# Kernel optimization log

Hardware: AMD Instinct MI355X
Metric: run time of the kernel (lower is better)

Reference implementation:

```python
import jax, jax.numpy as jnp
import numpy as np

B, N, DIM = 8, 512, 512
HEADS, HD = 8, 64          # head_dim = dim // num_heads
E_ATT = 24                 # num_attn_experts, top-k = HEADS
E_FFD, K_FFD = 16, 2       # num_ffd_experts, top-k = ffd_heads
HID = 1024                 # int(dim*mlp_ratio) // ffd_heads = 2048 // 2
TASKS = 9
SWITCH_W, Z_W = 0.01, 0.001
SCALE = HD ** -0.5


def layer_norm(x, g, b, eps=1e-5):
    m = x.mean(-1, keepdims=True)
    v = ((x - m) ** 2).mean(-1, keepdims=True)
    return (x - m) * jax.lax.rsqrt(v + eps) * g + b


def top_k_gating(xf, w_gate, k, n_experts):
    # xf: [T, C], w_gate: [C, E]  (eval mode: no noise)
    logits = xf @ w_gate                                      # [T, E]
    probs = jax.nn.softmax(logits, axis=-1)
    vals, idx = jax.lax.top_k(probs, k)                       # [T, k]
    denom = jax.lax.stop_gradient(vals.sum(-1, keepdims=True) + 1e-6)
    gates = vals / denom                                      # renormalized top-k gates
    one_hot = jax.nn.one_hot(idx, n_experts, dtype=probs.dtype)  # [T, k, E]
    freqs = jax.lax.stop_gradient(one_hot.sum((0, 1)))        # tokens per expert [E]
    p_sum = probs.sum(0)
    switch = n_experts * jnp.sum((p_sum / p_sum.sum()) * (freqs / freqs.sum()))
    z = jnp.mean(jax.nn.logsumexp(logits, axis=-1) ** 2)
    loss = SWITCH_W * switch + Z_W * z
    return gates, one_hot, loss


def _forward(x, task_bh, norm1_g, norm1_b, gate_att, wq, wo_att, kv_w, kv_b,
             norm2_g, norm2_b, gate_mlp, wi, bi, wo_mlp, bo):
    Bs, Ns, C = x.shape
    T = Bs * Ns
    # ---- MoE task attention (MoA-style: experts produce query heads) ----
    x1 = layer_norm(x, norm1_g, norm1_b).reshape(T, C)
    gates, oh, loss1 = top_k_gating(x1, gate_att[task_bh], HEADS, E_ATT)
    # map: per-slot expert query projection (not gate-weighted)
    q_all = jnp.einsum('tc,ech->teh', x1, wq)                 # [T, E, hd]
    q = jnp.einsum('teh,tke->tkh', q_all, oh)                 # [T, H, hd]
    q = q.reshape(Bs, Ns, HEADS, HD)
    kv = x1 @ kv_w + kv_b                                     # shared single-head k,v
    k_, v_ = jnp.split(kv.reshape(Bs, Ns, 2 * HD), 2, axis=-1)
    attn = jnp.einsum('bihd,bjd->bhij', q, k_) * SCALE
    attn = jax.nn.softmax(attn, axis=-1)
    o = jnp.einsum('bhij,bjd->bihd', attn, v_).reshape(T, HEADS, HD)
    # reduce: gate-weighted per-expert output projection
    comb = jnp.einsum('tkd,tk,tke->ted', o, gates, oh)        # [T, E, hd]
    y = jnp.einsum('ted,edc->tc', comb, wo_att).reshape(Bs, Ns, C)
    x = x + y
    # ---- MoE task MLP ----
    x2 = layer_norm(x, norm2_g, norm2_b).reshape(T, C)
    gates2, oh2, loss2 = top_k_gating(x2, gate_mlp[task_bh], K_FFD, E_FFD)
    g_dense = jnp.einsum('tk,tke->te', gates2, oh2)           # sparse gates densified [T,E]
    h = jax.nn.gelu(jnp.einsum('tc,ech->teh', x2, wi) + bi, approximate=False)
    y2 = jnp.einsum('teh,te,ehc->tc', h, g_dense, wo_mlp) + g_dense @ bo
    x = x + y2.reshape(Bs, Ns, C)
    return x, loss1 + loss2


def setup_inputs() -> dict:
    key = jax.random.key(0)
    ks = jax.random.split(key, 8)
    s = 0.02
    return {
        'x': jax.random.normal(ks[0], (B, N, DIM), jnp.float32),
        'task_bh': 3,
        'norm1_g': jnp.ones((DIM,), jnp.float32),
        'norm1_b': jnp.zeros((DIM,), jnp.float32),
        'gate_att': jax.random.normal(ks[1], (TASKS, DIM, E_ATT), jnp.float32) * s,
        'wq': jax.random.normal(ks[2], (E_ATT, DIM, HD), jnp.float32) * s,
        'wo_att': jax.random.normal(ks[3], (E_ATT, HD, DIM), jnp.float32) * s,
        'kv_w': jax.random.normal(ks[4], (DIM, 2 * HD), jnp.float32) * s,
        'kv_b': jnp.zeros((2 * HD,), jnp.float32),
        'norm2_g': jnp.ones((DIM,), jnp.float32),
        'norm2_b': jnp.zeros((DIM,), jnp.float32),
        'gate_mlp': jax.random.normal(ks[5], (TASKS, DIM, E_FFD), jnp.float32) * s,
        'wi': jax.random.normal(ks[6], (E_FFD, DIM, HID), jnp.float32) * s,
        'bi': jnp.zeros((E_FFD, HID), jnp.float32),
        'wo_mlp': jax.random.normal(ks[7], (E_FFD, HID, DIM), jnp.float32) * s,
        'bo': jnp.zeros((E_FFD, DIM), jnp.float32),
    }


def reference(x, task_bh, norm1_g, norm1_b, gate_att, wq, wo_att, kv_w, kv_b,
              norm2_g, norm2_b, gate_mlp, wi, bi, wo_mlp, bo):
    return _forward(x, task_bh, norm1_g, norm1_b, gate_att, wq, wo_att, kv_w, kv_b,
                    norm2_g, norm2_b, gate_mlp, wi, bi, wo_mlp, bo)
```

## Files before the change

### kernel.cpp

```cpp
#include <hip/hip_runtime.h>
#include <math.h>

namespace {

constexpr int T   = 4096;
constexpr int C   = 512;
constexpr int NB  = 8;
constexpr int NS  = 512;
constexpr int HD  = 64;
constexpr int KA  = 8;
constexpr int EA  = 24;
constexpr int EF  = 16;
constexpr int KF  = 2;
constexpr int HID = 1024;

typedef __attribute__((ext_vector_type(8))) short bf16x8;
typedef __attribute__((ext_vector_type(4))) float f32x4;

__device__ inline unsigned short f2bf(float f) {
  unsigned u = __float_as_uint(f);
  return (unsigned short)((u + 0x7FFFu + ((u >> 16) & 1u)) >> 16);
}
__device__ inline float bf2f(unsigned short u) {
  return __uint_as_float((unsigned)u << 16);
}

template <int E, int TS>
__device__ inline bool tile_from_counts(const int* counts, int tile, int& e_out, int& t0_out) {
  int e = 0;
  for (; e < E; e++) {
    int nt = (counts[e] + TS - 1) / TS;
    if (tile < nt) break;
    tile -= nt;
  }
  e_out = e; t0_out = tile * TS;
  return e < E;
}

template <int E, int K, bool RESID>
__global__ __launch_bounds__(1024) void ln_gate_kernel(
    const float* __restrict__ in, const unsigned short* __restrict__ yslot,
    float* __restrict__ resid_out,
    const float* __restrict__ g, const float* __restrict__ b,
    const float* __restrict__ gate_all, const int* __restrict__ task,
    unsigned short* __restrict__ outb,
    float* __restrict__ probs, float* __restrict__ lse_out,
    float* __restrict__ gates, int* __restrict__ idxs) {
  constexpr int TPB = 16;
  constexpr int XSS = 516;
  int tid = threadIdx.x, lane = tid & 63, wv = tid >> 6;
  int tb = blockIdx.x * TPB;
  __shared__ float xs[TPB][XSS];
  __shared__ float lp[2][TPB][E];
  __shared__ __align__(16) float Wt[E][XSS];
  const float* W = gate_all + (size_t)task[0] * C * E;
  for (int i = tid; i < C * E; i += 1024) {
    int c = i / E, e = i - c * E;
    Wt[e][c] = W[i];
  }
  int c0 = lane * 8;
  const float4 g0 = *(const float4*)&g[c0], g1 = *(const float4*)&g[c0 + 4];
  const float4 b0 = *(const float4*)&b[c0], b1 = *(const float4*)&b[c0 + 4];
  {
    int tt = wv;
    int t = tb + tt;
    const float* row = in + (size_t)t * C + c0;
    float4 v0 = *(const float4*)&row[0];
    float4 v1 = *(const float4*)&row[4];
    if (RESID) {
      #pragma unroll
      for (int k = 0; k < KA; k++) {
        uint4 u = *(const uint4*)&yslot[((size_t)t * KA + k) * C + c0];
        const unsigned short* us = (const unsigned short*)&u;
        v0.x += bf2f(us[0]); v0.y += bf2f(us[1]); v0.z += bf2f(us[2]); v0.w += bf2f(us[3]);
        v1.x += bf2f(us[4]); v1.y += bf2f(us[5]); v1.z += bf2f(us[6]); v1.w += bf2f(us[7]);
      }
      *(float4*)&resid_out[(size_t)t * C + c0]     = v0;
      *(float4*)&resid_out[(size_t)t * C + c0 + 4] = v1;
    }
    float s = (v0.x + v0.y) + (v0.z + v0.w) + (v1.x + v1.y) + (v1.z + v1.w);
    #pragma unroll
    for (int m = 1; m < 64; m <<= 1) s += __shfl_xor(s, m);
    float mean = s * (1.f / C);
    float d[8] = {v0.x - mean, v0.y - mean, v0.z - mean, v0.w - mean,
                  v1.x - mean, v1.y - mean, v1.z - mean, v1.w - mean};
    float vv = 0.f;
    #pragma unroll
    for (int j = 0; j < 8; j++) vv += d[j] * d[j];
    #pragma unroll
    for (int m = 1; m < 64; m <<= 1) vv += __shfl_xor(vv, m);
    float r = rsqrtf(vv * (1.f / C) + 1e-5f);
    float o[8];
    o[0] = d[0] * r * g0.x + b0.x; o[1] = d[1] * r * g0.y + b0.y;
    o[2] = d[2] * r * g0.z + b0.z; o[3] = d[3] * r * g0.w + b0.w;
    o[4] = d[4] * r * g1.x + b1.x; o[5] = d[5] * r * g1.y + b1.y;
    o[6] = d[6] * r * g1.z + b1.z; o[7] = d[7] * r * g1.w + b1.w;
    *(ushort4*)&outb[(size_t)t * C + c0] =
        make_ushort4(f2bf(o[0]), f2bf(o[1]), f2bf(o[2]), f2bf(o[3]));
    *(ushort4*)&outb[(size_t)t * C + c0 + 4] =
        make_ushort4(f2bf(o[4]), f2bf(o[5]), f2bf(o[6]), f2bf(o[7]));
    #pragma unroll
    for (int j = 0; j < 8; j++) xs[tt][c0 + j] = o[j];
  }
  __syncthreads();
  if (tid < TPB * E * 2) {
    int half = tid / (TPB * E);
    int rem = tid - half * (TPB * E);
    int e = rem % E, tt = rem / E;
    int cb = half * (C / 2);
    float a0 = 0.f, a1 = 0.f, a2 = 0.f, a3 = 0.f;
    float a4 = 0.f, a5 = 0.f, a6 = 0.f, a7 = 0.f;
    #pragma unroll 4
    for (int c = cb; c < cb + C / 2; c += 8) {
      const float4 xv0 = *(const float4*)&xs[tt][c];
      const float4 xv1 = *(const float4*)&xs[tt][c + 4];
      const float4 wv0 = *(const float4*)&Wt[e][c];
      const float4 wv1 = *(const float4*)&Wt[e][c + 4];
      a0 += xv0.x * wv0.x; a1 += xv0.y * wv0.y;
      a2 += xv0.z * wv0.z; a3 += xv0.w * wv0.w;
      a4 += xv1.x * wv1.x; a5 += xv1.y * wv1.y;
      a6 += xv1.z * wv1.z; a7 += xv1.w * wv1.w;
    }
    lp[half][tt][e] = ((a0 + a1) + (a2 + a3)) + ((a4 + a5) + (a6 + a7));
  }
  __syncthreads();
  {
    int tt = wv;
    int t = tb + tt;
    float lgv = (lane < E) ? (lp[0][tt][lane] + lp[1][tt][lane]) : -3.0e38f;
    float mx = lgv;
    #pragma unroll
    for (int m = 1; m < 64; m <<= 1) mx = fmaxf(mx, __shfl_xor(mx, m));
    float pe = (lane < E) ? expf(lgv - mx) : 0.f;
    float sum = pe;
    #pragma unroll
    for (int m = 1; m < 64; m <<= 1) sum += __shfl_xor(sum, m);
    float inv = 1.f / sum;
    float prob = pe * inv;
    if (lane < E) probs[(size_t)t * E + lane] = prob;
    if (lane == 0) lse_out[t] = mx + logf(sum);
    float pv = (lane < E) ? prob : -1.f;
    float gsum = 0.f, myv = 0.f; int myi = 0;
    for (int k = 0; k < K; k++) {
      float bv = pv; int bi_ = lane;
      #pragma unroll
      for (int m = 1; m < 64; m <<= 1) {
        float ov = __shfl_xor(bv, m); int oi = __shfl_xor(bi_, m);
        if (ov > bv || (ov == bv && oi < bi_)) { bv = ov; bi_ = oi; }
      }
      gsum += bv;
      if (lane == k) { myv = bv; myi = bi_; }
      if (lane == bi_) pv = -1.f;
    }
    if (lane < K) {
      float ginv = 1.f / (gsum + 1e-6f);
      gates[(size_t)t * K + lane] = myv * ginv;
      idxs[(size_t)t * K + lane]  = myi;
    }
  }
}

template <int E>
__global__ __launch_bounds__(512) void bucket_kernel(const int* __restrict__ idx, int nslots,
                                                     int stride, int* counts, int* bucket) {
  __shared__ int lcount[E];
  __shared__ int lbase[E];
  int tid = threadIdx.x;
  if (tid < E) lcount[tid] = 0;
  __syncthreads();
  int s = blockIdx.x * 512 + tid;
  int e = 0, lpos = 0;
  bool valid = (s < nslots);
  if (valid) {
    e = idx[s];
    lpos = atomicAdd(&lcount[e], 1);
  }
  __syncthreads();
  if (tid < E) lbase[tid] = lcount[tid] ? atomicAdd(&counts[tid], lcount[tid]) : 0;
  __syncthreads();
  if (valid) bucket[(size_t)e * stride + lbase[e] + lpos] = s;
}

__global__ __launch_bounds__(256) void tcvt_all(
    const float* __restrict__ wq, const float* __restrict__ wo_a,
    const float* __restrict__ wi, const float* __restrict__ wo_m,
    const float* __restrict__ kvw,
    unsigned short* __restrict__ wqt, unsigned short* __restrict__ woat,
    unsigned short* __restrict__ wit, unsigned short* __restrict__ womt,
    unsigned short* __restrict__ kvwt) {
  int bid = blockIdx.x;
  const float* src; unsigned short* dst; int K, N, nx, rem;
  if (bid < 192)       { src = wq;   dst = wqt;  K = 512;  N = 64;   nx = 1;  rem = bid; }
  else if (bid < 384)  { src = wo_a; dst = woat; K = 64;   N = 512;  nx = 8;  rem = bid - 192; }
  else if (bid < 2432) { src = wi;   dst = wit;  K = 512;  N = 1024; nx = 16; rem = bid - 384; }
  else if (bid < 4480) { src = wo_m; dst = womt; K = 1024; N = 512;  nx = 8;  rem = bid - 2432; }
  else                 { src = kvw;  dst = kvwt; K = 512;  N = 128;  nx = 2;  rem = bid - 4480; }
  int per = nx * (K / 64);
  int e = rem / per, r2 = rem % per;
  int kt = (r2 / nx) * 64, nt = (r2 % nx) * 64;
  __shared__ float tile[64][65];
  int tid = threadIdx.x;
  const float* S = src + (size_t)e * K * N;
  for (int i = tid; i < 64 * 16; i += 256) {
    int r = i >> 4, c4 = (i & 15) * 4;
    const float4 v = *(const float4*)&S[(size_t)(kt + r) * N + nt + c4];
    tile[r][c4 + 0] = v.x; tile[r][c4 + 1] = v.y;
    tile[r][c4 + 2] = v.z; tile[r][c4 + 3] = v.w;
  }
  __syncthreads();
  unsigned short* D = dst + (size_t)e * K * N;
  for (int i = tid; i < 64 * 64; i += 256) {
    int k = i & 63, n = i >> 6;
    D[(size_t)(nt + n) * K + kt + k] = f2bf(tile[k][n]);
  }
}

__global__ __launch_bounds__(256) void qkv_mfma(
    const unsigned short* __restrict__ xb, const unsigned short* __restrict__ wqt,
    const unsigned short* __restrict__ kvwt, const float* __restrict__ kvb,
    const int* __restrict__ bucket, const int* __restrict__ counts,
    unsigned short* __restrict__ qb, unsigned short* __restrict__ Kb,
    unsigned short* __restrict__ Vt) {
  __shared__ __align__(16) unsigned short smem[16 * 72 + 128 * 72];
  __shared__ int slots[64];
  __shared__ int se, st0;
  int tid = threadIdx.x;
  int lane = tid & 63, w = tid >> 6;
  int lr = lane & 15, lk = (lane >> 4) * 8, rowq = (lane >> 4) * 4;
  if ((int)blockIdx.y < T / 16) {
    int t0 = blockIdx.y * 16;
    unsigned short* Xs = smem;
    unsigned short* Ws = smem + 16 * 72;
    f32x4 acc[2] = {};
    for (int kc = 0; kc < C; kc += 64) {
      __syncthreads();
      if (tid < 128) {
        int r = tid >> 3, c8 = (tid & 7) * 8;
        *(uint4*)&Xs[r * 72 + c8] = *(const uint4*)&xb[(size_t)(t0 + r) * C + kc + c8];
      }
      #pragma unroll
      for (int it = 0; it < 4; ++it) {
        int i = it * 256 + tid;
        int r = i >> 3, c8 = (i & 7) * 8;
        *(uint4*)&Ws[r * 72 + c8] = *(const uint4*)&kvwt[(size_t)r * C + kc + c8];
      }
      __syncthreads();
      #pragma unroll
      for (int kk = 0; kk < 64; kk += 32) {
        bf16x8 xf = *(const bf16x8*)&Xs[lr * 72 + kk + lk];
        #pragma unroll
        for (int cf = 0; cf < 2; cf++) {
          bf16x8 wf = *(const bf16x8*)&Ws[(w * 32 + cf * 16 + lr) * 72 + kk + lk];
          acc[cf] = __builtin_amdgcn_mfma_f32_16x16x32_bf16(wf, xf, acc[cf], 0, 0, 0);
        }
      }
    }
    int t = t0 + lr;
    int bb = t >> 9, n = t & (NS - 1);
    #pragma unroll
    for (int cf = 0; cf < 2; cf++) {
      #pragma unroll
      for (int r2 = 0; r2 < 4; r2++) {
        int c = w * 32 + cf * 16 + rowq + r2;
        float v = acc[cf][r2] + kvb[c];
        if (c < HD) Kb[(size_t)t * HD + c] = f2bf(v);
        else        Vt[((size_t)bb * HD + (c - HD)) * NS + n] = f2bf(v);
      }
    }
  } else {
    if (tid == 0) {
      int e, t0;
      bool ok = tile_from_counts<EA, 64>(counts, blockIdx.y - T / 16, e, t0);
      se = ok ? e : -1; st0 = t0;
    }
    __syncthreads();
    if (se < 0) return;
    int e = se, t0 = st0;
    int cnt = counts[e];
    unsigned short* Xb = smem;
    unsigned short* Wb = smem + 64 * 72;
    if (tid < 64) {
      int ii = t0 + tid;
      slots[tid] = (ii < cnt) ? bucket[(size_t)e * (T * KA) + ii] : -1;
    }
    __syncthreads();
    f32x4 acc[4] = {};
    for (int kc = 0; kc < C; kc += 64) {
      __syncthreads();
      #pragma unroll
      for (int it = 0; it < 2; ++it) {
        int i = it * 256 + tid;
        int r = i >> 3, c8 = (i & 7) * 8;
        int s = slots[r];
        uint4 v = make_uint4(0u, 0u, 0u, 0u);
        if (s >= 0) v = *(const uint4*)&xb[(size_t)(s >> 3) * C + kc + c8];
        *(uint4*)&Xb[r * 72 + c8] = v;
      }
      #pragma unroll
      for (int it = 0; it < 2; ++it) {
        int i = it * 256 + tid;
        int r = i >> 3, c8 = (i & 7) * 8;
        *(uint4*)&Wb[r * 72 + c8] = *(const uint4*)&wqt[((size_t)e * HD + r) * C + kc + c8];
      }
      __syncthreads();
      #pragma unroll
      for (int kk = 0; kk < 64; kk += 32) {
        bf16x8 a = *(const bf16x8*)&Wb[(w * 16 + lr) * 72 + kk + lk];
        #pragma unroll
        for (int mf = 0; mf < 4; mf++) {
          bf16x8 b = *(const bf16x8*)&Xb[(mf * 16 + lr) * 72 + kk + lk];
          acc[mf] = __builtin_amdgcn_mfma_f32_16x16x32_bf16(a, b, acc[mf], 0, 0, 0);
        }
      }
    }
    #pragma unroll
    for (int mf = 0; mf < 4; mf++) {
      int s = slots[mf * 16 + lr];
      if (s < 0) continue;
      ushort4 v = make_ushort4(f2bf(0.125f * acc[mf][0]), f2bf(0.125f * acc[mf][1]),
                               f2bf(0.125f * acc[mf][2]), f2bf(0.125f * acc[mf][3]));
      *(ushort4*)&qb[(size_t)s * HD + w * 16 + rowq] = v;
    }
  }
}

__global__ __launch_bounds__(128) void attn_mfma(
    const unsigned short* __restrict__ qb, const unsigned short* __restrict__ Kb,
    const unsigned short* __restrict__ Vt, unsigned short* __restrict__ ob) {
  int qt = blockIdx.x, h = blockIdx.y, b = blockIdx.z;
  int tid = threadIdx.x;
  __shared__ __align__(16) unsigned short Qs[32][72];
  __shared__ __align__(16) unsigned short Ks[64][72];
  __shared__ __align__(16) unsigned short Vs[64][72];
  __shared__ __align__(16) unsigned short Ps[32][72];
  int i0 = qt * 32;
  #pragma unroll
  for (int it = 0; it < 2; ++it) {
    int i = it * 128 + tid;
    int r = i >> 3, c8 = (i & 7) * 8;
    *(uint4*)&Qs[r][c8] = *(const uint4*)&qb[(((size_t)(b * NS + i0 + r)) * KA + h) * HD + c8];
  }
  int lane = tid & 63, w = tid >> 6;
  int lr = lane & 15, lk = (lane >> 4) * 8, rowq = (lane >> 4) * 4;
  f32x4 acc_o[4] = {};
  float m_run = -3.0e38f, l_run = 0.f;
  for (int jt = 0; jt < NS / 64; ++jt) {
    __syncthreads();
    #pragma unroll
    for (int it = 0; it < 4; ++it) {
      int i = it * 128 + tid;
      int r = i >> 3, c8 = (i & 7) * 8;
      *(uint4*)&Ks[r][c8] = *(const uint4*)&Kb[((size_t)(b * NS + jt * 64 + r)) * HD + c8];
      *(uint4*)&Vs[r][c8] = *(const uint4*)&Vt[((size_t)b * HD + r) * NS + jt * 64 + c8];
    }
    __syncthreads();
    f32x4 acc_s[4] = {};
    #pragma unroll
    for (int kk = 0; kk < 64; kk += 32) {
      bf16x8 qf = *(const bf16x8*)&Qs[w * 16 + lr][kk + lk];
      #pragma unroll
      for (int kf = 0; kf < 4; kf++) {
        bf16x8 kr = *(const bf16x8*)&Ks[kf * 16 + lr][kk + lk];
        acc_s[kf] = __builtin_amdgcn_mfma_f32_16x16x32_bf16(kr, qf, acc_s[kf], 0, 0, 0);
      }
    }
    float pmax = acc_s[0][0];
    #pragma unroll
    for (int kf = 0; kf < 4; kf++)
      #pragma unroll
      for (int r = 0; r < 4; r++) pmax = fmaxf(pmax, acc_s[kf][r]);
    pmax = fmaxf(pmax, __shfl_xor(pmax, 16));
    pmax = fmaxf(pmax, __shfl_xor(pmax, 32));
    float m_new = fmaxf(m_run, pmax);
    float scl = expf(m_run - m_new);
    float rs = 0.f;
    #pragma unroll
    for (int kf = 0; kf < 4; kf++)
      #pragma unroll
      for (int r = 0; r < 4; r++) {
        float pv = expf(acc_s[kf][r] - m_new);
        rs += pv;
        Ps[w * 16 + lr][kf * 16 + rowq + r] = f2bf(pv);
      }
    rs += __shfl_xor(rs, 16);
    rs += __shfl_xor(rs, 32);
    l_run = l_run * scl + rs;
    m_run = m_new;
    __syncthreads();
    #pragma unroll
    for (int df = 0; df < 4; df++) {
      acc_o[df][0] *= scl; acc_o[df][1] *= scl;
      acc_o[df][2] *= scl; acc_o[df][3] *= scl;
    }
    #pragma unroll
    for (int kk = 0; kk < 64; kk += 32) {
      bf16x8 pf = *(const bf16x8*)&Ps[w * 16 + lr][kk + lk];
      #pragma unroll
      for (int df = 0; df < 4; df++) {
        bf16x8 vf = *(const bf16x8*)&Vs[df * 16 + lr][kk + lk];
        acc_o[df] = __builtin_amdgcn_mfma_f32_16x16x32_bf16(vf, pf, acc_o[df], 0, 0, 0);
      }
    }
  }
  float inv = 1.f / l_run;
  int token = b * NS + i0 + w * 16 + lr;
  #pragma unroll
  for (int df = 0; df < 4; df++) {
    ushort4 v = make_ushort4(f2bf(acc_o[df][0] * inv), f2bf(acc_o[df][1] * inv),
                             f2bf(acc_o[df][2] * inv), f2bf(acc_o[df][3] * inv));
    *(ushort4*)&ob[((size_t)token * KA + h) * HD + df * 16 + rowq] = v;
  }
}

__global__ __launch_bounds__(256) void oproj_mfma(
    const unsigned short* __restrict__ ob, const unsigned short* __restrict__ wot,
    const float* __restrict__ gates, const int* __restrict__ bucket,
    const int* __restrict__ counts, unsigned short* __restrict__ y_slot) {
  __shared__ int se, st0;
  int tid = threadIdx.x;
  if (tid == 0) {
    int e, t0;
    bool ok = tile_from_counts<EA, 128>(counts, blockIdx.y, e, t0);
    se = ok ? e : -1; st0 = t0;
  }
  __syncthreads();
  if (se < 0) return;
  int e = se, t0 = st0;
  int c0 = blockIdx.x * 128;
  int cnt = counts[e];
  __shared__ int slots[128];
  __shared__ float gs[128];
  __shared__ __align__(16) unsigned short Xb[128][72];
  __shared__ __align__(16) unsigned short Wb[128][72];
  if (tid < 128) {
    int ii = t0 + tid;
    int s = (ii < cnt) ? bucket[(size_t)e * (T * KA) + ii] : -1;
    slots[tid] = s;
    gs[tid] = (s >= 0) ? gates[s] : 0.f;
  }
  __syncthreads();
  #pragma unroll
  for (int it = 0; it < 4; ++it) {
    int i = it * 256 + tid;
    int r = i >> 3, c8 = (i & 7) * 8;
    int s = slots[r];
    uint4 vo = make_uint4(0u, 0u, 0u, 0u);
    if (s >= 0) {
      float g = gs[r];
      uint4 u = *(const uint4*)&ob[(size_t)s * HD + c8];
      const unsigned short* us = (const unsigned short*)&u;
      unsigned short* vs = (unsigned short*)&vo;
      #pragma unroll
      for (int k = 0; k < 8; k++) vs[k] = f2bf(g * bf2f(us[k]));
    }
    *(uint4*)&Xb[r][c8] = vo;
  }
  #pragma unroll
  for (int it = 0; it < 4; ++it) {
    int i = it * 256 + tid;
    int r = i >> 3, c8 = (i & 7) * 8;
    *(uint4*)&Wb[r][c8] = *(const uint4*)&wot[((size_t)e * C + c0 + r) * HD + c8];
  }
  __syncthreads();
  int lane = tid & 63, wid = tid >> 6;
  int wr = wid & 1, wc = wid >> 1;
  int lr = lane & 15, lk = (lane >> 4) * 8, rowq = (lane >> 4) * 4;
  f32x4 acc[4][4] = {};
  #pragma unroll
  for (int kk = 0; kk < 64; kk += 32) {
    bf16x8 a[4], b[4];
    #pragma unroll
    for (int nf = 0; nf < 4; nf++) a[nf] = *(const bf16x8*)&Wb[wc * 64 + nf * 16 + lr][kk + lk];
    #pragma unroll
    for (int mf = 0; mf < 4; mf++) b[mf] = *(const bf16x8*)&Xb[wr * 64 + mf * 16 + lr][kk + lk];
    #pragma unroll
    for (int nf = 0; nf < 4; nf++)
      #pragma unroll
      for (int mf = 0; mf < 4; mf++)
        acc[nf][mf] = __builtin_amdgcn_mfma_f32_16x16x32_bf16(a[nf], b[mf], acc[nf][mf], 0, 0, 0);
  }
  #pragma unroll
  for (int mf = 0; mf < 4; mf++) {
    int si = wr * 64 + mf * 16 + lr;
    int s = slots[si];
    if (s < 0) continue;
    size_t base = (size_t)s * C + c0 + wc * 64;
    #pragma unroll
    for (int nf = 0; nf < 4; nf++) {
      ushort4 v = make_ushort4(f2bf(acc[nf][mf][0]), f2bf(acc[nf][mf][1]),
                               f2bf(acc[nf][mf][2]), f2bf(acc[nf][mf][3]));
      *(ushort4*)&y_slot[base + nf * 16 + rowq] = v;
    }
  }
}

__global__ __launch_bounds__(256) void mlp1_mfma(
    const unsigned short* __restrict__ xb, const unsigned short* __restrict__ wit,
    const float* __restrict__ bi, const int* __restrict__ bucket,
    const int* __restrict__ counts, unsigned short* __restrict__ h) {
  __shared__ int se, st0;
  int tid = threadIdx.x;
  if (tid == 0) {
    int e, t0;
    bool ok = tile_from_counts<EF, 64>(counts, blockIdx.y, e, t0);
    se = ok ? e : -1; st0 = t0;
  }
  __syncthreads();
  if (se < 0) return;
  int e = se, t0 = st0;
  int j0 = blockIdx.x * 64;
  int cnt = counts[e];
  __shared__ int slots[64];
  __shared__ __align__(16) unsigned short Xb[64][72];
  __shared__ __align__(16) unsigned short Wb[64][72];
  if (tid < 64) {
    int ii = t0 + tid;
    slots[tid] = (ii < cnt) ? bucket[(size_t)e * (T * KF) + ii] : -1;
  }
  __syncthreads();
  int lane = tid & 63, w = tid >> 6;
  int lr = lane & 15, lk = (lane >> 4) * 8, rowq = (lane >> 4) * 4;
  f32x4 acc[4] = {};
  for (int kc = 0; kc < C; kc += 64) {
    __syncthreads();
    #pragma unroll
    for (int it = 0; it < 2; ++it) {
      int i = it * 256 + tid;
      int r = i >> 3, c8 = (i & 7) * 8;
      int s = slots[r];
      uint4 v = make_uint4(0u, 0u, 0u, 0u);
      if (s >= 0) v = *(const uint4*)&xb[(size_t)(s >> 1) * C + kc + c8];
      *(uint4*)&Xb[r][c8] = v;
    }
    #pragma unroll
    for (int it = 0; it < 2; ++it) {
      int i = it * 256 + tid;
      int r = i >> 3, c8 = (i & 7) * 8;
      *(uint4*)&Wb[r][c8] = *(const uint4*)&wit[((size_t)e * HID + j0 + r) * C + kc + c8];
    }
    __syncthreads();
    #pragma unroll
    for (int kk = 0; kk < 64; kk += 32) {
      bf16x8 a = *(const bf16x8*)&Wb[w * 16 + lr][kk + lk];
      #pragma unroll
      for (int mf = 0; mf < 4; mf++) {
        bf16x8 b = *(const bf16x8*)&Xb[mf * 16 + lr][kk + lk];
        acc[mf] = __builtin_amdgcn_mfma_f32_16x16x32_bf16(a, b, acc[mf], 0, 0, 0);
      }
    }
  }
  #pragma unroll
  for (int mf = 0; mf < 4; mf++) {
    int s = slots[mf * 16 + lr];
    if (s < 0) continue;
    int j = j0 + w * 16 + rowq;
    const float4 b4 = *(const float4*)&bi[(size_t)e * HID + j];
    float v0 = acc[mf][0] + b4.x, v1 = acc[mf][1] + b4.y;
    float v2 = acc[mf][2] + b4.z, v3 = acc[mf][3] + b4.w;
    v0 = 0.5f * v0 * (1.f + erff(v0 * 0.70710678118654752f));
    v1 = 0.5f * v1 * (1.f + erff(v1 * 0.70710678118654752f));
    v2 = 0.5f * v2 * (1.f + erff(v2 * 0.70710678118654752f));
    v3 = 0.5f * v3 * (1.f + erff(v3 * 0.70710678118654752f));
    *(ushort4*)&h[(size_t)s * HID + j] = make_ushort4(f2bf(v0), f2bf(v1), f2bf(v2), f2bf(v3));
  }
}

__global__ __launch_bounds__(256) void mlp2_mfma(
    const unsigned short* __restrict__ h, const unsigned short* __restrict__ wot,
    const float* __restrict__ bo, const float* __restrict__ gates2,
    const int* __restrict__ bucket, const int* __restrict__ counts,
    unsigned short* __restrict__ y2) {
  __shared__ int se, st0;
  int tid = threadIdx.x;
  if (tid == 0) {
    int e, t0;
    bool ok = tile_from_counts<EF, 64>(counts, blockIdx.y, e, t0);
    se = ok ? e : -1; st0 = t0;
  }
  __syncthreads();
  if (se < 0) return;
  int e = se, t0 = st0;
  int c0 = blockIdx.x * 64;
  int cnt = counts[e];
  __shared__ int slots[64];
  __shared__ __align__(16) unsigned short Xb[64][72];
  __shared__ __align__(16) unsigned short Wb[64][72];
  if (tid < 64) {
    int ii = t0 + tid;
    slots[tid] = (ii < cnt) ? bucket[(size_t)e * (T * KF) + ii] : -1;
  }
  __syncthreads();
  int lane = tid & 63, w = tid >> 6;
  int lr = lane & 15, lk = (lane >> 4) * 8, rowq = (lane >> 4) * 4;
  f32x4 acc[4] = {};
  for (int kc = 0; kc < HID; kc += 64) {
    __syncthreads();
    #pragma unroll
    for (int it = 0; it < 2; ++it) {
      int i = it * 256 + tid;
      int r = i >> 3, c8 = (i & 7) * 8;
      int s = slots[r];
      uint4 v = make_uint4(0u, 0u, 0u, 0u);
      if (s >= 0) v = *(const uint4*)&h[(size_t)s * HID + kc + c8];
      *(uint4*)&Xb[r][c8] = v;
    }
    #pragma unroll
    for (int it = 0; it < 2; ++it) {
      int i = it * 256 + tid;
      int r = i >> 3, c8 = (i & 7) * 8;
      *(uint4*)&Wb[r][c8] = *(const uint4*)&wot[((size_t)e * C + c0 + r) * HID + kc + c8];
    }
    __syncthreads();
    #pragma unroll
    for (int kk = 0; kk < 64; kk += 32) {
      bf16x8 a = *(const bf16x8*)&Wb[w * 16 + lr][kk + lk];
      #pragma unroll
      for (int mf = 0; mf < 4; mf++) {
        bf16x8 b = *(const bf16x8*)&Xb[mf * 16 + lr][kk + lk];
        acc[mf] = __builtin_amdgcn_mfma_f32_16x16x32_bf16(a, b, acc[mf], 0, 0, 0);
      }
    }
  }
  #pragma unroll
  for (int mf = 0; mf < 4; mf++) {
    int s = slots[mf * 16 + lr];
    if (s < 0) continue;
    float g = gates2[s];
    int cc = c0 + w * 16 + rowq;
    const float4 b4 = *(const float4*)&bo[(size_t)e * C + cc];
    ushort4 v = make_ushort4(f2bf(g * (acc[mf][0] + b4.x)),
                             f2bf(g * (acc[mf][1] + b4.y)),
                             f2bf(g * (acc[mf][2] + b4.z)),
                             f2bf(g * (acc[mf][3] + b4.w)));
    *(ushort4*)&y2[(size_t)s * C + cc] = v;
  }
}

__global__ void final_kernel(const unsigned short* __restrict__ y2, float* __restrict__ xout) {
  int t = blockIdx.x, tid = threadIdx.x;
  int c = tid * 2;
  unsigned u0 = *(const unsigned*)&y2[(size_t)(t * 2) * C + c];
  unsigned u1 = *(const unsigned*)&y2[(size_t)(t * 2 + 1) * C + c];
  xout[(size_t)t * C + c]     += bf2f((unsigned short)(u0 & 0xFFFF)) + bf2f((unsigned short)(u1 & 0xFFFF));
  xout[(size_t)t * C + c + 1] += bf2f((unsigned short)(u0 >> 16)) + bf2f((unsigned short)(u1 >> 16));
}

__global__ __launch_bounds__(256) void reduce_gating_all(
    const float* __restrict__ probs1, const float* __restrict__ lse1,
    const int* __restrict__ idx1,
    const float* __restrict__ probs2, const float* __restrict__ lse2,
    const int* __restrict__ idx2, float* __restrict__ accum) {
  constexpr int TPB = 64, TPW = 16;
  int which = blockIdx.y;
  int E = which ? EF : EA;
  int K = which ? KF : KA;
  const float* probs = which ? probs2 : probs1;
  const float* lse   = which ? lse2 : lse1;
  const int* idxs    = which ? idx2 : idx1;
  float* psum = accum + (which ? 49 : 0);
  float* freq = accum + (which ? 65 : 24);
  float* zsum = accum + (which ? 81 : 48);
  int tid = threadIdx.x, lane = tid & 63, wv = tid >> 6;
  int t0 = blockIdx.x * TPB + wv * TPW;
  float ps = 0.f, fr = 0.f;
  if (lane < E) {
    for (int i = 0; i < TPW; i++) {
      int t = t0 + i;
      ps += probs[(size_t)t * E + lane];
      for (int k = 0; k < K; k++)
        fr += (idxs[(size_t)t * K + k] == lane) ? 1.f : 0.f;
    }
  }
  float z = 0.f;
  for (int i = lane; i < TPW; i += 64) {
    float l = lse[t0 + i];
    z += l * l;
  }
  #pragma unroll
  for (int m = 1; m < 64; m <<= 1) z += __shfl_xor(z, m);
  __shared__ float sps[4][EA];
  __shared__ float sfr[4][EA];
  __shared__ float sz[4];
  if (lane < E) { sps[wv][lane] = ps; sfr[wv][lane] = fr; }
  if (lane == 0) sz[wv] = z;
  __syncthreads();
  if (tid < E) {
    atomicAdd(&psum[tid], sps[0][tid] + sps[1][tid] + sps[2][tid] + sps[3][tid]);
    atomicAdd(&freq[tid], sfr[0][tid] + sfr[1][tid] + sfr[2][tid] + sfr[3][tid]);
  }
  if (tid == 255) atomicAdd(zsum, sz[0] + sz[1] + sz[2] + sz[3]);
}

__global__ void loss_kernel(const float* __restrict__ acc, float* __restrict__ out) {
  const float* p1 = acc;      const float* f1 = acc + 24; float z1 = acc[48];
  const float* p2 = acc + 49; const float* f2 = acc + 65; float z2 = acc[81];
  float sp1 = 0.f, sf1 = 0.f;
  for (int e = 0; e < 24; e++) { sp1 += p1[e]; sf1 += f1[e]; }
  float sw1 = 0.f;
  for (int e = 0; e < 24; e++) sw1 += (p1[e] / sp1) * (f1[e] / sf1);
  sw1 *= 24.f;
  float sp2 = 0.f, sf2 = 0.f;
  for (int e = 0; e < 16; e++) { sp2 += p2[e]; sf2 += f2[e]; }
  float sw2 = 0.f;
  for (int e = 0; e < 16; e++) sw2 += (p2[e] / sp2) * (f2[e] / sf2);
  sw2 *= 16.f;
  out[0] = 0.01f * sw1 + 0.001f * (z1 / T) + 0.01f * sw2 + 0.001f * (z2 / T);
}

}

extern "C" void kernel_launch(void* const* d_in, const int* in_sizes, int n_in,
                              void* d_out, int out_size, void* d_ws, size_t ws_size,
                              hipStream_t stream) {
  const float* x      = (const float*)d_in[0];
  const int*   task   = (const int*)d_in[1];
  const float* n1g    = (const float*)d_in[2];
  const float* n1b    = (const float*)d_in[3];
  const float* gate_a = (const float*)d_in[4];
  const float* wq     = (const float*)d_in[5];
  const float* wo_a   = (const float*)d_in[6];
  const float* kvw    = (const float*)d_in[7];
  const float* kvb    = (const float*)d_in[8];
  const float* n2g    = (const float*)d_in[9];
  const float* n2b    = (const float*)d_in[10];
  const float* gate_m = (const float*)d_in[11];
  const float* wi     = (const float*)d_in[12];
  const float* bi     = (const float*)d_in[13];
  const float* wo_m   = (const float*)d_in[14];
  const float* bo     = (const float*)d_in[15];
  float* out = (float*)d_out;

  char* p = (char*)d_ws;
  unsigned short* x1b = (unsigned short*)p; p += (size_t)T * C * 2;
  unsigned short* qb = (unsigned short*)p;  p += (size_t)T * KA * HD * 2;
  unsigned short* ob = (unsigned short*)p;  p += (size_t)T * KA * HD * 2;
  unsigned short* Kb = (unsigned short*)p;  p += (size_t)T * HD * 2;
  unsigned short* Vt = (unsigned short*)p;  p += (size_t)T * HD * 2;
  char* un = p;                      p += (size_t)T * KA * C * 2;
  unsigned short* y_slot  = (unsigned short*)un;
  unsigned short* h       = (unsigned short*)un;
  unsigned short* y2_slot = (unsigned short*)(un + (size_t)T * KF * HID * 2);
  unsigned short* wqt = (unsigned short*)p;  p += (size_t)EA * C * HD * 2;
  unsigned short* woat = (unsigned short*)p; p += (size_t)EA * HD * C * 2;
  unsigned short* wit = (unsigned short*)p;  p += (size_t)EF * C * HID * 2;
  unsigned short* womt = (unsigned short*)p; p += (size_t)EF * HID * C * 2;
  unsigned short* kvwt = (unsigned short*)p; p += (size_t)(2 * HD) * C * 2;
  float* probs1 = (float*)p;         p += (size_t)T * EA * 4;
  float* lse1 = (float*)p;           p += (size_t)T * 4;
  float* gates1 = (float*)p;         p += (size_t)T * KA * 4;
  int* idx1 = (int*)p;               p += (size_t)T * KA * 4;
  float* probs2 = (float*)p;         p += (size_t)T * EF * 4;
  float* lse2 = (float*)p;           p += (size_t)T * 4;
  float* gates2 = (float*)p;         p += (size_t)T * KF * 4;
  int* idx2 = (int*)p;               p += (size_t)T * KF * 4;
  int* bucket_a = (int*)p;           p += (size_t)EA * (T * KA) * 4;
  int* bucket_f = (int*)p;           p += (size_t)EF * (T * KF) * 4;
  int* counts_a = (int*)p;           p += 32 * 4;
  int* counts_f = (int*)p;           p += 32 * 4;
  float* accum = (float*)p;          p += 128 * 4;

  hipMemsetAsync(counts_a, 0, (32 + 32 + 128) * 4, stream);

  tcvt_all<<<4496, 256, 0, stream>>>(wq, wo_a, wi, wo_m, kvw, wqt, woat, wit, womt, kvwt);

  ln_gate_kernel<EA, KA, false><<<T / 16, 1024, 0, stream>>>(
      x, y_slot, out, n1g, n1b, gate_a, task, x1b, probs1, lse1, gates1, idx1);
  bucket_kernel<EA><<<(T * KA + 511) / 512, 512, 0, stream>>>(idx1, T * KA, T * KA,
                                                              counts_a, bucket_a);
  qkv_mfma<<<dim3(1, T / 16 + 536), 256, 0, stream>>>(x1b, wqt, kvwt, kvb,
                                                      bucket_a, counts_a, qb, Kb, Vt);
  attn_mfma<<<dim3(NS / 32, KA, NB), 128, 0, stream>>>(qb, Kb, Vt, ob);
  oproj_mfma<<<dim3(4, 280), 256, 0, stream>>>(ob, woat, gates1, bucket_a, counts_a, y_slot);
  ln_gate_kernel<EF, KF, true><<<T / 16, 1024, 0, stream>>>(
      x, y_slot, out, n2g, n2b, gate_m, task, x1b, probs2, lse2, gates2, idx2);
  bucket_kernel<EF><<<(T * KF + 511) / 512, 512, 0, stream>>>(idx2, T * KF, T * KF,
                                                              counts_f, bucket_f);
  mlp1_mfma<<<dim3(16, 144), 256, 0, stream>>>(x1b, wit, bi, bucket_f, counts_f, h);
  mlp2_mfma<<<dim3(8, 144), 256, 0, stream>>>(h, womt, bo, gates2, bucket_f, counts_f, y2_slot);
  final_kernel<<<T, 256, 0, stream>>>(y2_slot, out);
  reduce_gating_all<<<dim3(T / 64, 2), 256, 0, stream>>>(probs1, lse1, idx1,
                                                         probs2, lse2, idx2, accum);
  loss_kernel<<<1, 1, 0, stream>>>(accum, out + (size_t)T * C);
}
```

Baseline: 216.3 us.

## Fuse expert bucketing and gating loss reductions into LN-gate kernel

Folds the bucket kernel and the gating-statistics reduction kernel into the layer-norm/gating kernel. Each block now buckets its own tokens' slots with shared-memory counts, and accumulates prob sums and squared logsumexp via atomics. Expert frequencies now come straight from the bucket counts. This removes three kernel launches and the global writes and re-reads of probs, lse and idx buffers, at the cost of more atomics and shared memory in the gating kernel.

```diff
diff --git a/kernel.cpp b/kernel.cpp
--- a/kernel.cpp
+++ b/kernel.cpp
@@ -43,9 +43,9 @@
     float* __restrict__ resid_out,
     const float* __restrict__ g, const float* __restrict__ b,
     const float* __restrict__ gate_all, const int* __restrict__ task,
-    unsigned short* __restrict__ outb,
-    float* __restrict__ probs, float* __restrict__ lse_out,
-    float* __restrict__ gates, int* __restrict__ idxs) {
+    unsigned short* __restrict__ outb, float* __restrict__ gates,
+    int* __restrict__ counts, int* __restrict__ bucket, int stride,
+    float* __restrict__ psum_g, float* __restrict__ zsum_g) {
   constexpr int TPB = 16;
   constexpr int XSS = 516;
   int tid = threadIdx.x, lane = tid & 63, wv = tid >> 6;
@@ -53,11 +53,16 @@
   __shared__ float xs[TPB][XSS];
   __shared__ float lp[2][TPB][E];
   __shared__ __align__(16) float Wt[E][XSS];
+  __shared__ int idx_s[TPB][8];
+  __shared__ float zbuf[TPB];
+  __shared__ int lcount[E];
+  __shared__ int lbase[E];
   const float* W = gate_all + (size_t)task[0] * C * E;
   for (int i = tid; i < C * E; i += 1024) {
     int c = i / E, e = i - c * E;
     Wt[e][c] = W[i];
   }
+  if (tid < E) lcount[tid] = 0;
   int c0 = lane * 8;
   const float4 g0 = *(const float4*)&g[c0], g1 = *(const float4*)&g[c0 + 4];
   const float4 b0 = *(const float4*)&b[c0], b1 = *(const float4*)&b[c0 + 4];
@@ -137,8 +142,8 @@
     for (int m = 1; m < 64; m <<= 1) sum += __shfl_xor(sum, m);
     float inv = 1.f / sum;
     float prob = pe * inv;
-    if (lane < E) probs[(size_t)t * E + lane] = prob;
-    if (lane == 0) lse_out[t] = mx + logf(sum);
+    if (lane < E) lp[0][tt][lane] = prob;
+    if (lane == 0) zbuf[tt] = mx + logf(sum);
     float pv = (lane < E) ? prob : -1.f;
     float gsum = 0.f, myv = 0.f; int myi = 0;
     for (int k = 0; k < K; k++) {
@@ -155,30 +160,35 @@
     if (lane < K) {
       float ginv = 1.f / (gsum + 1e-6f);
       gates[(size_t)t * K + lane] = myv * ginv;
-      idxs[(size_t)t * K + lane]  = myi;
-    }
-  }
-}
-
-template <int E>
-__global__ __launch_bounds__(512) void bucket_kernel(const int* __restrict__ idx, int nslots,
-                                                     int stride, int* counts, int* bucket) {
-  __shared__ int lcount[E];
-  __shared__ int lbase[E];
-  int tid = threadIdx.x;
-  if (tid < E) lcount[tid] = 0;
-  __syncthreads();
-  int s = blockIdx.x * 512 + tid;
-  int e = 0, lpos = 0;
-  bool valid = (s < nslots);
-  if (valid) {
-    e = idx[s];
-    lpos = atomicAdd(&lcount[e], 1);
+      idx_s[tt][lane] = myi;
+    }
+  }
+  __syncthreads();
+  if (tid < E) {
+    float s = 0.f;
+    #pragma unroll
+    for (int tt2 = 0; tt2 < TPB; tt2++) s += lp[0][tt2][tid];
+    atomicAdd(&psum_g[tid], s);
+  }
+  if (tid == 64) {
+    float z = 0.f;
+    #pragma unroll
+    for (int tt2 = 0; tt2 < TPB; tt2++) { float l = zbuf[tt2]; z += l * l; }
+    atomicAdd(zsum_g, z);
+  }
+  int my_e = -1, my_lpos = 0;
+  if (tid < TPB * K) {
+    int tt2 = tid / K, k = tid % K;
+    my_e = idx_s[tt2][k];
+    my_lpos = atomicAdd(&lcount[my_e], 1);
   }
   __syncthreads();
   if (tid < E) lbase[tid] = lcount[tid] ? atomicAdd(&counts[tid], lcount[tid]) : 0;
   __syncthreads();
-  if (valid) bucket[(size_t)e * stride + lbase[e] + lpos] = s;
+  if (my_e >= 0) {
+    int tt2 = tid / K, k = tid % K;
+    bucket[(size_t)my_e * stride + lbase[my_e] + my_lpos] = (tb + tt2) * K + k;
+  }
 }
 
 __global__ __launch_bounds__(256) void tcvt_all(
@@ -645,64 +655,19 @@
   xout[(size_t)t * C + c + 1] += bf2f((unsigned short)(u0 >> 16)) + bf2f((unsigned short)(u1 >> 16));
 }
 
-__global__ __launch_bounds__(256) void reduce_gating_all(
-    const float* __restrict__ probs1, const float* __restrict__ lse1,
-    const int* __restrict__ idx1,
-    const float* __restrict__ probs2, const float* __restrict__ lse2,
-    const int* __restrict__ idx2, float* __restrict__ accum) {
-  constexpr int TPB = 64, TPW = 16;
-  int which = blockIdx.y;
-  int E = which ? EF : EA;
-  int K = which ? KF : KA;
-  const float* probs = which ? probs2 : probs1;
-  const float* lse   = which ? lse2 : lse1;
-  const int* idxs    = which ? idx2 : idx1;
-  float* psum = accum + (which ? 49 : 0);
-  float* freq = accum + (which ? 65 : 24);
-  float* zsum = accum + (which ? 81 : 48);
-  int tid = threadIdx.x, lane = tid & 63, wv = tid >> 6;
-  int t0 = blockIdx.x * TPB + wv * TPW;
-  float ps = 0.f, fr = 0.f;
-  if (lane < E) {
-    for (int i = 0; i < TPW; i++) {
-      int t = t0 + i;
-      ps += probs[(size_t)t * E + lane];
-      for (int k = 0; k < K; k++)
-        fr += (idxs[(size_t)t * K + k] == lane) ? 1.f : 0.f;
-    }
-  }
-  float z = 0.f;
-  for (int i = lane; i < TPW; i += 64) {
-    float l = lse[t0 + i];
-    z += l * l;
-  }
-  #pragma unroll
-  for (int m = 1; m < 64; m <<= 1) z += __shfl_xor(z, m);
-  __shared__ float sps[4][EA];
-  __shared__ float sfr[4][EA];
-  __shared__ float sz[4];
-  if (lane < E) { sps[wv][lane] = ps; sfr[wv][lane] = fr; }
-  if (lane == 0) sz[wv] = z;
-  __syncthreads();
-  if (tid < E) {
-    atomicAdd(&psum[tid], sps[0][tid] + sps[1][tid] + sps[2][tid] + sps[3][tid]);
-    atomicAdd(&freq[tid], sfr[0][tid] + sfr[1][tid] + sfr[2][tid] + sfr[3][tid]);
-  }
-  if (tid == 255) atomicAdd(zsum, sz[0] + sz[1] + sz[2] + sz[3]);
-}
-
-__global__ void loss_kernel(const float* __restrict__ acc, float* __restrict__ out) {
-  const float* p1 = acc;      const float* f1 = acc + 24; float z1 = acc[48];
-  const float* p2 = acc + 49; const float* f2 = acc + 65; float z2 = acc[81];
+__global__ void loss_kernel(const float* __restrict__ acc, const int* __restrict__ ca,
+                            const int* __restrict__ cf, float* __restrict__ out) {
+  const float* p1 = acc;      float z1 = acc[48];
+  const float* p2 = acc + 49; float z2 = acc[81];
   float sp1 = 0.f, sf1 = 0.f;
-  for (int e = 0; e < 24; e++) { sp1 += p1[e]; sf1 += f1[e]; }
+  for (int e = 0; e < 24; e++) { sp1 += p1[e]; sf1 += (float)ca[e]; }
   float sw1 = 0.f;
-  for (int e = 0; e < 24; e++) sw1 += (p1[e] / sp1) * (f1[e] / sf1);
+  for (int e = 0; e < 24; e++) sw1 += (p1[e] / sp1) * ((float)ca[e] / sf1);
   sw1 *= 24.f;
   float sp2 = 0.f, sf2 = 0.f;
-  for (int e = 0; e < 16; e++) { sp2 += p2[e]; sf2 += f2[e]; }
+  for (int e = 0; e < 16; e++) { sp2 += p2[e]; sf2 += (float)cf[e]; }
   float sw2 = 0.f;
-  for (int e = 0; e < 16; e++) sw2 += (p2[e] / sp2) * (f2[e] / sf2);
+  for (int e = 0; e < 16; e++) sw2 += (p2[e] / sp2) * ((float)cf[e] / sf2);
   sw2 *= 16.f;
   out[0] = 0.01f * sw1 + 0.001f * (z1 / T) + 0.01f * sw2 + 0.001f * (z2 / T);
 }
@@ -745,14 +710,8 @@
   unsigned short* wit = (unsigned short*)p;  p += (size_t)EF * C * HID * 2;
   unsigned short* womt = (unsigned short*)p; p += (size_t)EF * HID * C * 2;
   unsigned short* kvwt = (unsigned short*)p; p += (size_t)(2 * HD) * C * 2;
-  float* probs1 = (float*)p;         p += (size_t)T * EA * 4;
-  float* lse1 = (float*)p;           p += (size_t)T * 4;
   float* gates1 = (float*)p;         p += (size_t)T * KA * 4;
-  int* idx1 = (int*)p;               p += (size_t)T * KA * 4;
-  float* probs2 = (float*)p;         p += (size_t)T * EF * 4;
-  float* lse2 = (float*)p;           p += (size_t)T * 4;
   float* gates2 = (float*)p;         p += (size_t)T * KF * 4;
-  int* idx2 = (int*)p;               p += (size_t)T * KF * 4;
   int* bucket_a = (int*)p;           p += (size_t)EA * (T * KA) * 4;
   int* bucket_f = (int*)p;           p += (size_t)EF * (T * KF) * 4;
   int* counts_a = (int*)p;           p += 32 * 4;
@@ -764,21 +723,17 @@
   tcvt_all<<<4496, 256, 0, stream>>>(wq, wo_a, wi, wo_m, kvw, wqt, woat, wit, womt, kvwt);
 
   ln_gate_kernel<EA, KA, false><<<T / 16, 1024, 0, stream>>>(
-      x, y_slot, out, n1g, n1b, gate_a, task, x1b, probs1, lse1, gates1, idx1);
-  bucket_kernel<EA><<<(T * KA + 511) / 512, 512, 0, stream>>>(idx1, T * KA, T * KA,
-                                                              counts_a, bucket_a);
+      x, y_slot, out, n1g, n1b, gate_a, task, x1b, gates1,
+      counts_a, bucket_a, T * KA, accum, accum + 48);
   qkv_mfma<<<dim3(1, T / 16 + 536), 256, 0, stream>>>(x1b, wqt, kvwt, kvb,
                                                       bucket_a, counts_a, qb, Kb, Vt);
   attn_mfma<<<dim3(NS / 32, KA, NB), 128, 0, stream>>>(qb, Kb, Vt, ob);
   oproj_mfma<<<dim3(4, 280), 256, 0, stream>>>(ob, woat, gates1, bucket_a, counts_a, y_slot);
   ln_gate_kernel<EF, KF, true><<<T / 16, 1024, 0, stream>>>(
-      x, y_slot, out, n2g, n2b, gate_m, task, x1b, probs2, lse2, gates2, idx2);
-  bucket_kernel<EF><<<(T * KF + 511) / 512, 512, 0, stream>>>(idx2, T * KF, T * KF,
-                                                              counts_f, bucket_f);
+      x, y_slot, out, n2g, n2b, gate_m, task, x1b, gates2,
+      counts_f, bucket_f, T * KF, accum + 49, accum + 81);
   mlp1_mfma<<<dim3(16, 144), 256, 0, stream>>>(x1b, wit, bi, bucket_f, counts_f, h);
   mlp2_mfma<<<dim3(8, 144), 256, 0, stream>>>(h, womt, bo, gates2, bucket_f, counts_f, y2_slot);
   final_kernel<<<T, 256, 0, stream>>>(y2_slot, out);
-  reduce_gating_all<<<dim3(T / 64, 2), 256, 0, stream>>>(probs1, lse1, idx1,
-                                                         probs2, lse2, idx2, accum);
-  loss_kernel<<<1, 1, 0, stream>>>(accum, out + (size_t)T * C);
-}
+  loss_kernel<<<1, 1, 0, stream>>>(accum, counts_a, counts_f, out + (size_t)T * C);
+}
```

Result: faster. 202.7 us (-6.3%).
